# Kernel optimization log

Measured on AMD Instinct MI355X. Metric: run time of the kernel, lower is better.

The kernel has to match this reference:

```python
import jax, jax.numpy as jnp
import numpy as np

B, C, S = 32, 2048, 28   # batch, in_channels, spatial_size
M, Q = 4, 1              # number of RAEs, hidden units per RAE
LAMBDA = 1e-3            # ridge regularization for the ELM-style decoder solve
EPS = 1e-10              # lp_norm_layer eps


def setup_inputs() -> dict:
    key = jax.random.key(0)
    k1, k2 = jax.random.split(key)
    x = jax.random.normal(k1, (B, C, S, S), dtype=jnp.float32)
    # Random (seeded, untrained) encoder weights for the M randomized autoencoders.
    W = jax.random.normal(k2, (M, C, Q), dtype=jnp.float32)
    return {"x": x, "W": W}


def _pos_encoding(n, d, dtype):
    # Standard sinusoidal 1D positional encoding over the n=H*W pixel positions,
    # d = channel dim (RADAM adds it to the per-pixel feature vectors).
    pos = jnp.arange(n, dtype=dtype)[:, None]                 # (n, 1)
    i = jnp.arange(0, d, 2, dtype=dtype)                      # (d/2,)
    div = jnp.exp(-(i / d) * jnp.log(jnp.asarray(10000.0, dtype)))
    pe = jnp.zeros((n, d), dtype)
    pe = pe.at[:, 0::2].set(jnp.sin(pos * div))
    pe = pe.at[:, 1::2].set(jnp.cos(pos * div))
    return pe


def reference(x, W):
    # x: (B, C, H, W) feature maps; W: (M, C, Q) random encoder weights.
    b, c, h, w = x.shape
    n = h * w
    # lp_norm_layer: L2-normalize each channel's spatial map jointly over (H, W).
    norm = jnp.sqrt(jnp.sum(x * x, axis=(2, 3), keepdims=True))
    xn = x / jnp.maximum(norm, EPS)
    # Resize(spatial_size) is identity (input already at spatial_size); flatten.
    feats = xn.reshape(b, c, n).transpose(0, 2, 1)            # (B, N, C) pixels-as-samples
    pe = _pos_encoding(n, c, x.dtype)                         # (N, C)
    xp = feats + pe[None]                                     # pos-encoded input
    # Hidden activations of all M RAEs for all batch elements at once.
    hid = jax.nn.sigmoid(jnp.einsum('bnc,mcq->bmnq', xp, W))  # (B, M, N, Q)
    # Closed-form ridge (ELM) decoder: beta = (H^T H + lam I)^{-1} H^T X
    hth = jnp.einsum('bmnq,bmnp->bmqp', hid, hid)             # (B, M, Q, Q)
    htx = jnp.einsum('bmnq,bnc->bmqc', hid, xp)               # (B, M, Q, C)
    eye = LAMBDA * jnp.eye(Q, dtype=x.dtype)
    beta = jnp.linalg.solve(hth + eye, htx)                   # (B, M, Q, C)
    # Sum decoder weights over the M RAEs (the per-rae pooled += in the loop).
    pooled = jnp.nan_to_num(jnp.sum(beta, axis=1))            # (B, Q, C)
    return pooled
```

## Files before the change

### kernel.cpp

```cpp
#include <hip/hip_runtime.h>
#include <math.h>

#define BB 32
#define CC 2048
#define NN 784
#define NF4 196
#define MM 4
#define NCH 64
#define CPER (CC / NCH)
#define LAMBDA_ 1e-3f
#define EPS_ 1e-10f
#define LOG1E4 9.210340371976184f
#define NORMB (BB * CC / 4)
#define OUT_BLOCKS (BB * CC / 4)

__device__ __forceinline__ float wred(float v) {
#pragma unroll
  for (int off = 32; off > 0; off >>= 1) v += __shfl_down(v, off, 64);
  return v;
}

__global__ __launch_bounds__(256) void k_norm_w(const float* __restrict__ x,
                                                const float* __restrict__ W,
                                                float* __restrict__ inv_norm,
                                                float* __restrict__ Ws,
                                                float* __restrict__ peW) {
  int bid  = blockIdx.x;
  int wv   = threadIdx.x >> 6;
  int lane = threadIdx.x & 63;

  if (bid >= NORMB) {
    int n = bid - NORMB;
    int m = wv;
    float acc = 0.f;
    for (int c = lane; c < CC; c += 64) {
      float di  = __expf(-((float)(c & ~1) * (1.f / CC)) * LOG1E4);
      float arg = (float)n * di;
      float pe  = (c & 1) ? __cosf(arg) : __sinf(arg);
      acc += pe * W[m * CC + c];
    }
    acc = wred(acc);
    if (lane == 0) peW[m * NN + n] = acc;
    return;
  }

  int idx = bid * 4 + wv;
  int b = idx >> 11;
  int c = idx & (CC - 1);
  const float4* row = (const float4*)(x + (size_t)idx * NN);
  float4 v0 = row[lane];
  float4 v1 = row[lane + 64];
  float4 v2 = row[lane + 128];
  float4 v3 = (lane < (NF4 - 192)) ? row[lane + 192] : make_float4(0.f, 0.f, 0.f, 0.f);
  float ss = v0.x*v0.x + v0.y*v0.y + v0.z*v0.z + v0.w*v0.w
           + v1.x*v1.x + v1.y*v1.y + v1.z*v1.z + v1.w*v1.w
           + v2.x*v2.x + v2.y*v2.y + v2.z*v2.z + v2.w*v2.w
           + v3.x*v3.x + v3.y*v3.y + v3.z*v3.z + v3.w*v3.w;
  ss = wred(ss);
  if (lane == 0) {
    float inv = 1.f / fmaxf(sqrtf(ss), EPS_);
    inv_norm[idx] = inv;
#pragma unroll
    for (int m = 0; m < MM; ++m)
      Ws[((size_t)b * MM + m) * CC + c] = W[m * CC + c] * inv;
  }
}

__global__ __launch_bounds__(256, 8) void k_sacc5(const float* __restrict__ x,
                                                  const float* __restrict__ Ws,
                                                  float4* __restrict__ sPart4) {
  int t  = threadIdx.x;
  int ch = blockIdx.x;
  int b  = blockIdx.y;
  if (t >= NF4) return;
  int c0 = ch * CPER;
  const float4* xb = (const float4*)(x + ((size_t)b * CC + c0) * NN) + t;
  const float* wb  = Ws + (size_t)b * MM * CC + c0;

  float4 a0{0,0,0,0}, a1{0,0,0,0}, a2{0,0,0,0}, a3{0,0,0,0};

  for (int i = 0; i < CPER; i += 4) {
    float4 xv[4];
#pragma unroll
    for (int u = 0; u < 4; ++u) xv[u] = xb[(size_t)(i + u) * NF4];
#pragma unroll
    for (int u = 0; u < 4; ++u) {
      int c = i + u;
      float w0 = wb[0 * CC + c];
      float w1 = wb[1 * CC + c];
      float w2 = wb[2 * CC + c];
      float w3 = wb[3 * CC + c];
      float4 v = xv[u];
      a0.x += v.x * w0; a0.y += v.y * w0; a0.z += v.z * w0; a0.w += v.w * w0;
      a1.x += v.x * w1; a1.y += v.y * w1; a1.z += v.z * w1; a1.w += v.w * w1;
      a2.x += v.x * w2; a2.y += v.y * w2; a2.z += v.z * w2; a2.w += v.w * w2;
      a3.x += v.x * w3; a3.y += v.y * w3; a3.z += v.z * w3; a3.w += v.w * w3;
    }
  }
  size_t base = (((size_t)b * NCH + ch) * MM) * NF4 + t;
  sPart4[base + 0 * NF4] = a0;
  sPart4[base + 1 * NF4] = a1;
  sPart4[base + 2 * NF4] = a2;
  sPart4[base + 3 * NF4] = a3;
}

__global__ __launch_bounds__(256) void k_hid2(const float* __restrict__ sPart,
                                              const float* __restrict__ peW,
                                              float* __restrict__ hid4,
                                              float* __restrict__ aDpart) {
  int g = blockIdx.x;
  int b = blockIdx.y;
  int t = threadIdx.x;
  int n = g * 256 + t;
  bool valid = n < NN;
  int wv = t >> 6, lane = t & 63;

  float h[MM];
#pragma unroll
  for (int m = 0; m < MM; ++m) {
    float hm = 0.f;
    if (valid) {
      float s = peW[m * NN + n];
#pragma unroll 8
      for (int ch = 0; ch < NCH; ++ch)
        s += sPart[(((size_t)b * NCH + ch) * MM + m) * NN + n];
      hm = 1.f / (1.f + __expf(-s));
    }
    h[m] = hm;
  }
  if (valid) {
    float4 hv = make_float4(h[0], h[1], h[2], h[3]);
    *(float4*)(hid4 + ((size_t)b * NN + n) * 4) = hv;
  }

  __shared__ float red[4][MM];
#pragma unroll
  for (int m = 0; m < MM; ++m) {
    float q = wred(h[m] * h[m]);
    if (lane == 0) red[wv][m] = q;
  }
  __syncthreads();
  if (t < MM)
    aDpart[((size_t)b * 4 + g) * MM + t] = red[0][t] + red[1][t] + red[2][t] + red[3][t];
}

__global__ __launch_bounds__(256) void k_out3(const float* __restrict__ x,
                                              const float* __restrict__ hid4,
                                              const float* __restrict__ inv_norm,
                                              const float* __restrict__ aDpart,
                                              float* __restrict__ out) {
  int idx  = blockIdx.x * 4 + (threadIdx.x >> 6);
  int lane = threadIdx.x & 63;
  int b = idx >> 11;
  int c = idx & (CC - 1);
  const float4* row = (const float4*)(x + (size_t)idx * NN);
  const float4* hb  = (const float4*)(hid4 + (size_t)b * NN * 4);
  float di = __expf(-((float)(c & ~1) * (1.0f / CC)) * LOG1E4);
  bool use_sin = !(c & 1);
  float aX0=0,aX1=0,aX2=0,aX3=0, aP0=0,aP1=0,aP2=0,aP3=0;
  for (int f = lane; f < NF4; f += 64) {
    float4 xv = row[f];
    int n = f * 4;
    float4 h0 = hb[n + 0], h1 = hb[n + 1], h2 = hb[n + 2], h3 = hb[n + 3];
    float a0 = (float)(n + 0) * di, a1 = (float)(n + 1) * di;
    float a2 = (float)(n + 2) * di, a3 = (float)(n + 3) * di;
    float p0 = use_sin ? __sinf(a0) : __cosf(a0);
    float p1 = use_sin ? __sinf(a1) : __cosf(a1);
    float p2 = use_sin ? __sinf(a2) : __cosf(a2);
    float p3 = use_sin ? __sinf(a3) : __cosf(a3);
    aX0 += xv.x*h0.x + xv.y*h1.x + xv.z*h2.x + xv.w*h3.x;
    aX1 += xv.x*h0.y + xv.y*h1.y + xv.z*h2.y + xv.w*h3.y;
    aX2 += xv.x*h0.z + xv.y*h1.z + xv.z*h2.z + xv.w*h3.z;
    aX3 += xv.x*h0.w + xv.y*h1.w + xv.z*h2.w + xv.w*h3.w;
    aP0 += p0*h0.x + p1*h1.x + p2*h2.x + p3*h3.x;
    aP1 += p0*h0.y + p1*h1.y + p2*h2.y + p3*h3.y;
    aP2 += p0*h0.z + p1*h1.z + p2*h2.z + p3*h3.z;
    aP3 += p0*h0.w + p1*h1.w + p2*h2.w + p3*h3.w;
  }
  aX0 = wred(aX0); aX1 = wred(aX1); aX2 = wred(aX2); aX3 = wred(aX3);
  aP0 = wred(aP0); aP1 = wred(aP1); aP2 = wred(aP2); aP3 = wred(aP3);
  if (lane == 0) {
    const float* ad = aDpart + (size_t)b * 4 * MM;
    float aD0 = ad[0] + ad[4] + ad[8]  + ad[12];
    float aD1 = ad[1] + ad[5] + ad[9]  + ad[13];
    float aD2 = ad[2] + ad[6] + ad[10] + ad[14];
    float aD3 = ad[3] + ad[7] + ad[11] + ad[15];
    float inv = inv_norm[idx];
    float r = (inv * aX0 + aP0) / (aD0 + LAMBDA_)
            + (inv * aX1 + aP1) / (aD1 + LAMBDA_)
            + (inv * aX2 + aP2) / (aD2 + LAMBDA_)
            + (inv * aX3 + aP3) / (aD3 + LAMBDA_);
    if (isnan(r)) r = 0.f;
    else if (isinf(r)) r = (r > 0.f) ? 3.4028234663852886e38f : -3.4028234663852886e38f;
    out[idx] = r;
  }
}

extern "C" void kernel_launch(void* const* d_in, const int* in_sizes, int n_in,
                              void* d_out, int out_size, void* d_ws, size_t ws_size,
                              hipStream_t stream) {
  const float* x = (const float*)d_in[0];
  const float* W = (const float*)d_in[1];
  float* out = (float*)d_out;
  float* ws  = (float*)d_ws;

  float* inv_norm = ws;
  float* peW      = inv_norm + (size_t)BB * CC;
  float* hid4     = peW + (size_t)MM * NN;
  float* Ws       = hid4 + (size_t)BB * NN * MM;
  float* aDpart   = Ws + (size_t)BB * MM * CC;
  float* sPart    = aDpart + (size_t)BB * 4 * MM;

  k_norm_w<<<NORMB + NN, 256, 0, stream>>>(x, W, inv_norm, Ws, peW);
  k_sacc5<<<dim3(NCH, BB), 256, 0, stream>>>(x, Ws, (float4*)sPart);
  k_hid2<<<dim3(4, BB), 256, 0, stream>>>(sPart, peW, hid4, aDpart);
  k_out3<<<OUT_BLOCKS, 256, 0, stream>>>(x, hid4, inv_norm, aDpart, out);
}
```

Before: 166.0 us.

## Store normalized input as fp16 once and reuse it in later passes

The norm kernel now writes an L2-normalized fp16 copy of x, so the accumulation and output kernels read half-size data instead of the fp32 input. The accumulation kernel uses raw W directly, since normalization is already applied, and the inv_norm and scaled-weight buffers are removed. The channel split is halved and the unroll is doubled. This cuts memory traffic on the two later passes in exchange for an extra fp16 write and reduced input precision.

```diff
diff --git a/kernel.cpp b/kernel.cpp
--- a/kernel.cpp
+++ b/kernel.cpp
@@ -1,12 +1,13 @@
 #include <hip/hip_runtime.h>
+#include <hip/hip_fp16.h>
 #include <math.h>
 
 #define BB 32
 #define CC 2048
 #define NN 784
-#define NF4 196
+#define NH4 196
 #define MM 4
-#define NCH 64
+#define NCH 32
 #define CPER (CC / NCH)
 #define LAMBDA_ 1e-3f
 #define EPS_ 1e-10f
@@ -14,16 +15,17 @@
 #define NORMB (BB * CC / 4)
 #define OUT_BLOCKS (BB * CC / 4)
 
+struct alignas(8) half4_t { __half2 lo, hi; };
+
 __device__ __forceinline__ float wred(float v) {
 #pragma unroll
   for (int off = 32; off > 0; off >>= 1) v += __shfl_down(v, off, 64);
   return v;
 }
 
-__global__ __launch_bounds__(256) void k_norm_w(const float* __restrict__ x,
+__global__ __launch_bounds__(256) void k_norm_h(const float* __restrict__ x,
                                                 const float* __restrict__ W,
-                                                float* __restrict__ inv_norm,
-                                                float* __restrict__ Ws,
+                                                half4_t* __restrict__ xh,
                                                 float* __restrict__ peW) {
   int bid  = blockIdx.x;
   int wv   = threadIdx.x >> 6;
@@ -45,63 +47,73 @@
   }
 
   int idx = bid * 4 + wv;
-  int b = idx >> 11;
-  int c = idx & (CC - 1);
   const float4* row = (const float4*)(x + (size_t)idx * NN);
   float4 v0 = row[lane];
   float4 v1 = row[lane + 64];
   float4 v2 = row[lane + 128];
-  float4 v3 = (lane < (NF4 - 192)) ? row[lane + 192] : make_float4(0.f, 0.f, 0.f, 0.f);
+  float4 v3 = (lane < 4) ? row[lane + 192] : make_float4(0.f, 0.f, 0.f, 0.f);
   float ss = v0.x*v0.x + v0.y*v0.y + v0.z*v0.z + v0.w*v0.w
            + v1.x*v1.x + v1.y*v1.y + v1.z*v1.z + v1.w*v1.w
            + v2.x*v2.x + v2.y*v2.y + v2.z*v2.z + v2.w*v2.w
            + v3.x*v3.x + v3.y*v3.y + v3.z*v3.z + v3.w*v3.w;
-  ss = wred(ss);
-  if (lane == 0) {
-    float inv = 1.f / fmaxf(sqrtf(ss), EPS_);
-    inv_norm[idx] = inv;
-#pragma unroll
-    for (int m = 0; m < MM; ++m)
-      Ws[((size_t)b * MM + m) * CC + c] = W[m * CC + c] * inv;
-  }
-}
-
-__global__ __launch_bounds__(256, 8) void k_sacc5(const float* __restrict__ x,
-                                                  const float* __restrict__ Ws,
-                                                  float4* __restrict__ sPart4) {
+#pragma unroll
+  for (int o = 1; o < 64; o <<= 1) ss += __shfl_xor(ss, o, 64);
+  float inv = 1.f / fmaxf(sqrtf(ss), EPS_);
+
+  half4_t* orow = xh + (size_t)idx * NH4;
+  half4_t p;
+  p.lo = __floats2half2_rn(v0.x * inv, v0.y * inv);
+  p.hi = __floats2half2_rn(v0.z * inv, v0.w * inv);
+  orow[lane] = p;
+  p.lo = __floats2half2_rn(v1.x * inv, v1.y * inv);
+  p.hi = __floats2half2_rn(v1.z * inv, v1.w * inv);
+  orow[lane + 64] = p;
+  p.lo = __floats2half2_rn(v2.x * inv, v2.y * inv);
+  p.hi = __floats2half2_rn(v2.z * inv, v2.w * inv);
+  orow[lane + 128] = p;
+  if (lane < 4) {
+    p.lo = __floats2half2_rn(v3.x * inv, v3.y * inv);
+    p.hi = __floats2half2_rn(v3.z * inv, v3.w * inv);
+    orow[lane + 192] = p;
+  }
+}
+
+__global__ __launch_bounds__(256) void k_sacc6(const half4_t* __restrict__ xh,
+                                               const float* __restrict__ W,
+                                               float4* __restrict__ sPart4) {
   int t  = threadIdx.x;
   int ch = blockIdx.x;
   int b  = blockIdx.y;
-  if (t >= NF4) return;
+  if (t >= NH4) return;
   int c0 = ch * CPER;
-  const float4* xb = (const float4*)(x + ((size_t)b * CC + c0) * NN) + t;
-  const float* wb  = Ws + (size_t)b * MM * CC + c0;
+  const half4_t* xb = xh + ((size_t)b * CC + c0) * NH4 + t;
 
   float4 a0{0,0,0,0}, a1{0,0,0,0}, a2{0,0,0,0}, a3{0,0,0,0};
 
-  for (int i = 0; i < CPER; i += 4) {
-    float4 xv[4];
-#pragma unroll
-    for (int u = 0; u < 4; ++u) xv[u] = xb[(size_t)(i + u) * NF4];
-#pragma unroll
-    for (int u = 0; u < 4; ++u) {
-      int c = i + u;
-      float w0 = wb[0 * CC + c];
-      float w1 = wb[1 * CC + c];
-      float w2 = wb[2 * CC + c];
-      float w3 = wb[3 * CC + c];
-      float4 v = xv[u];
-      a0.x += v.x * w0; a0.y += v.y * w0; a0.z += v.z * w0; a0.w += v.w * w0;
-      a1.x += v.x * w1; a1.y += v.y * w1; a1.z += v.z * w1; a1.w += v.w * w1;
-      a2.x += v.x * w2; a2.y += v.y * w2; a2.z += v.z * w2; a2.w += v.w * w2;
-      a3.x += v.x * w3; a3.y += v.y * w3; a3.z += v.z * w3; a3.w += v.w * w3;
+  for (int i = 0; i < CPER; i += 8) {
+    half4_t xv[8];
+#pragma unroll
+    for (int u = 0; u < 8; ++u) xv[u] = xb[(size_t)(i + u) * NH4];
+#pragma unroll
+    for (int u = 0; u < 8; ++u) {
+      int c = c0 + i + u;
+      float w0 = W[0 * CC + c];
+      float w1 = W[1 * CC + c];
+      float w2 = W[2 * CC + c];
+      float w3 = W[3 * CC + c];
+      float2 lo = __half22float2(xv[u].lo);
+      float2 hi = __half22float2(xv[u].hi);
+      a0.x += lo.x * w0; a0.y += lo.y * w0; a0.z += hi.x * w0; a0.w += hi.y * w0;
+      a1.x += lo.x * w1; a1.y += lo.y * w1; a1.z += hi.x * w1; a1.w += hi.y * w1;
+      a2.x += lo.x * w2; a2.y += lo.y * w2; a2.z += hi.x * w2; a2.w += hi.y * w2;
+      a3.x += lo.x * w3; a3.y += lo.y * w3; a3.z += hi.x * w3; a3.w += hi.y * w3;
     }
   }
-  size_t base = (((size_t)b * NCH + ch) * MM) * NF4 + t;
-  sPart4[base + 0 * NF4] = a0;
-  sPart4[base + 1 * NF4] = a1;
-  sPart4[base + 2 * NF4] = a2;
-  sPart4[base + 3 * NF4] = a3;
+  size_t base = (((size_t)b * NCH + ch) * MM) * NH4 + t;
+  sPart4[base + 0 * NH4] = a0;
+  sPart4[base + 1 * NH4] = a1;
+  sPart4[base + 2 * NH4] = a2;
+  sPart4[base + 3 * NH4] = a3;
 }
 
 __global__ __launch_bounds__(256) void k_hid2(const float* __restrict__ sPart,
@@ -144,22 +156,23 @@
     aDpart[((size_t)b * 4 + g) * MM + t] = red[0][t] + red[1][t] + red[2][t] + red[3][t];
 }
 
-__global__ __launch_bounds__(256) void k_out3(const float* __restrict__ x,
+__global__ __launch_bounds__(256) void k_out4(const half4_t* __restrict__ xh,
                                               const float* __restrict__ hid4,
-                                              const float* __restrict__ inv_norm,
                                               const float* __restrict__ aDpart,
                                               float* __restrict__ out) {
   int idx  = blockIdx.x * 4 + (threadIdx.x >> 6);
   int lane = threadIdx.x & 63;
   int b = idx >> 11;
   int c = idx & (CC - 1);
-  const float4* row = (const float4*)(x + (size_t)idx * NN);
-  const float4* hb  = (const float4*)(hid4 + (size_t)b * NN * 4);
+  const half4_t* row = xh + (size_t)idx * NH4;
+  const float4* hb   = (const float4*)(hid4 + (size_t)b * NN * 4);
   float di = __expf(-((float)(c & ~1) * (1.0f / CC)) * LOG1E4);
   bool use_sin = !(c & 1);
   float aX0=0,aX1=0,aX2=0,aX3=0, aP0=0,aP1=0,aP2=0,aP3=0;
-  for (int f = lane; f < NF4; f += 64) {
-    float4 xv = row[f];
+  for (int f = lane; f < NH4; f += 64) {
+    half4_t xv = row[f];
+    float2 lo = __half22float2(xv.lo);
+    float2 hi = __half22float2(xv.hi);
     int n = f * 4;
     float4 h0 = hb[n + 0], h1 = hb[n + 1], h2 = hb[n + 2], h3 = hb[n + 3];
     float a0 = (float)(n + 0) * di, a1 = (float)(n + 1) * di;
@@ -168,10 +181,10 @@
     float p1 = use_sin ? __sinf(a1) : __cosf(a1);
     float p2 = use_sin ? __sinf(a2) : __cosf(a2);
     float p3 = use_sin ? __sinf(a3) : __cosf(a3);
-    aX0 += xv.x*h0.x + xv.y*h1.x + xv.z*h2.x + xv.w*h3.x;
-    aX1 += xv.x*h0.y + xv.y*h1.y + xv.z*h2.y + xv.w*h3.y;
-    aX2 += xv.x*h0.z + xv.y*h1.z + xv.z*h2.z + xv.w*h3.z;
-    aX3 += xv.x*h0.w + xv.y*h1.w + xv.z*h2.w + xv.w*h3.w;
+    aX0 += lo.x*h0.x + lo.y*h1.x + hi.x*h2.x + hi.y*h3.x;
+    aX1 += lo.x*h0.y + lo.y*h1.y + hi.x*h2.y + hi.y*h3.y;
+    aX2 += lo.x*h0.z + lo.y*h1.z + hi.x*h2.z + hi.y*h3.z;
+    aX3 += lo.x*h0.w + lo.y*h1.w + hi.x*h2.w + hi.y*h3.w;
     aP0 += p0*h0.x + p1*h1.x + p2*h2.x + p3*h3.x;
     aP1 += p0*h0.y + p1*h1.y + p2*h2.y + p3*h3.y;
     aP2 += p0*h0.z + p1*h1.z + p2*h2.z + p3*h3.z;
@@ -185,11 +198,10 @@
     float aD1 = ad[1] + ad[5] + ad[9]  + ad[13];
     float aD2 = ad[2] + ad[6] + ad[10] + ad[14];
     float aD3 = ad[3] + ad[7] + ad[11] + ad[15];
-    float inv = inv_norm[idx];
-    float r = (inv * aX0 + aP0) / (aD0 + LAMBDA_)
-            + (inv * aX1 + aP1) / (aD1 + LAMBDA_)
-            + (inv * aX2 + aP2) / (aD2 + LAMBDA_)
-            + (inv * aX3 + aP3) / (aD3 + LAMBDA_);
+    float r = (aX0 + aP0) / (aD0 + LAMBDA_)
+            + (aX1 + aP1) / (aD1 + LAMBDA_)
+            + (aX2 + aP2) / (aD2 + LAMBDA_)
+            + (aX3 + aP3) / (aD3 + LAMBDA_);
     if (isnan(r)) r = 0.f;
     else if (isinf(r)) r = (r > 0.f) ? 3.4028234663852886e38f : -3.4028234663852886e38f;
     out[idx] = r;
@@ -204,15 +216,14 @@
   float* out = (float*)d_out;
   float* ws  = (float*)d_ws;
 
-  float* inv_norm = ws;
-  float* peW      = inv_norm + (size_t)BB * CC;
-  float* hid4     = peW + (size_t)MM * NN;
-  float* Ws       = hid4 + (size_t)BB * NN * MM;
-  float* aDpart   = Ws + (size_t)BB * MM * CC;
-  float* sPart    = aDpart + (size_t)BB * 4 * MM;
-
-  k_norm_w<<<NORMB + NN, 256, 0, stream>>>(x, W, inv_norm, Ws, peW);
-  k_sacc5<<<dim3(NCH, BB), 256, 0, stream>>>(x, Ws, (float4*)sPart);
+  float* peW    = ws;
+  float* hid4   = peW + (size_t)MM * NN;
+  float* aDpart = hid4 + (size_t)BB * NN * MM;
+  float* sPart  = aDpart + (size_t)BB * 4 * MM;
+  half4_t* xh   = (half4_t*)(sPart + (size_t)BB * NCH * MM * NN);
+
+  k_norm_h<<<NORMB + NN, 256, 0, stream>>>(x, W, xh, peW);
+  k_sacc6<<<dim3(NCH, BB), 256, 0, stream>>>(xh, W, (float4*)sPart);
   k_hid2<<<dim3(4, BB), 256, 0, stream>>>(sPart, peW, hid4, aDpart);
-  k_out3<<<OUT_BLOCKS, 256, 0, stream>>>(x, hid4, inv_norm, aDpart, out);
-}
+  k_out4<<<OUT_BLOCKS, 256, 0, stream>>>(xh, hid4, aDpart, out);
+}
```

Result: faster. 155.0 us (-6.7%).
